# Kernel optimization log

Measured on AMD Instinct MI355X. Metric: run time of the kernel, lower is better.

## Reference

```python
import jax, jax.numpy as jnp
import numpy as np

N_NODES = 100000
N_EDGES = 3200000
D = 32


def _gat(x, edge_index, W, att_s, att_d, bias, heads, ch, neg_slope):
    """PyG-style GATConv (shared lin for src/dst, add_self_loops=False).
    x: [N, D_in], edge_index: [2, E], W: [heads*ch, D_in],
    att_s/att_d: [heads, ch], bias: [heads*ch]. Returns [N, heads*ch]."""
    n = x.shape[0]
    h = (x @ W.T).reshape(n, heads, ch)                      # [N,H,C]
    a_s = (h * att_s[None]).sum(-1)                           # [N,H]
    a_d = (h * att_d[None]).sum(-1)                           # [N,H]
    src, dst = edge_index[0], edge_index[1]
    logits = jax.nn.leaky_relu(a_s[src] + a_d[dst], neg_slope)  # [E,H]
    # segment softmax over edges grouped by destination node
    m = jax.ops.segment_max(logits, dst, num_segments=n)     # [N,H]
    m = jnp.where(jnp.isfinite(m), m, 0.0)                    # nodes w/ no in-edges
    ex = jnp.exp(logits - m[dst])                             # [E,H]
    denom = jax.ops.segment_sum(ex, dst, num_segments=n)     # [N,H]
    alpha = ex / (denom[dst] + 1e-16)                         # [E,H]
    out = jax.ops.segment_sum(alpha[:, :, None] * h[src], dst, num_segments=n)  # [N,H,C]
    return out.reshape(n, heads * ch) + bias


def setup_inputs() -> dict:
    key = jax.random.key(0)
    ks = jax.random.split(key, 16)
    x = jax.random.normal(ks[0], (N_NODES, D), dtype=jnp.float32)
    edge_index = jax.random.randint(ks[1], (2, N_EDGES), 0, N_NODES, dtype=jnp.int64)
    s = 1.0 / np.sqrt(D)
    return {
        "x": x,
        "edge_index": edge_index,
        "W1": jax.random.normal(ks[2], (32, D), dtype=jnp.float32) * s,
        "att_s1": jax.random.normal(ks[3], (2, 16), dtype=jnp.float32) * 0.05,
        "att_d1": jax.random.normal(ks[4], (2, 16), dtype=jnp.float32) * 0.05,
        "b1": jnp.full((32,), 0.1, dtype=jnp.float32),
        "ea1": jnp.ones((1,), dtype=jnp.float32),  # edge_activator
        "W2": jax.random.normal(ks[5], (32, 32), dtype=jnp.float32) * s,
        "att_s2": jax.random.normal(ks[6], (2, 16), dtype=jnp.float32) * 0.05,
        "att_d2": jax.random.normal(ks[7], (2, 16), dtype=jnp.float32) * 0.05,
        "b2": jnp.full((32,), 0.1, dtype=jnp.float32),
        "W3": jax.random.normal(ks[8], (32, 32), dtype=jnp.float32) * s,
        "att_s3": jax.random.normal(ks[9], (1, 32), dtype=jnp.float32) * 0.05,
        "att_d3": jax.random.normal(ks[10], (1, 32), dtype=jnp.float32) * 0.05,
        "b3": jnp.full((32,), 0.1, dtype=jnp.float32),
    }


def reference(x, edge_index, W1, att_s1, att_d1, b1, ea1,
              W2, att_s2, att_d2, b2, W3, att_s3, att_d3, b3):
    # --- layer 1 (negative_slope=0.01) ---
    h = _gat(x, edge_index, W1, att_s1, att_d1, b1, heads=2, ch=16, neg_slope=0.01)
    scale = jnp.tanh(ea1)[0]
    scale = jnp.where(scale < 0.1, 1.0, scale)  # 'continue' branch skips the scaling
    h = h * scale
    h = h + 0.05 * jax.lax.stop_gradient(h)      # h + 0.05*h.detach()
    h = jax.nn.elu(h)                            # eval path (training=False)
    h = jnp.clip(h, -3.0, 3.0)
    # --- layer 2 (default negative_slope=0.2) ---
    h = _gat(h, edge_index, W2, att_s2, att_d2, b2, heads=2, ch=16, neg_slope=0.2)
    h = jax.nn.elu(h)
    h = jnp.clip(h, -3.0, 3.0)
    # --- layer 3: heads=1, concat=False ---
    out = _gat(h, edge_index, W3, att_s3, att_d3, b3, heads=1, ch=32, neg_slope=0.2)
    return out
```

## Files before the change

kernel.cpp:

```cpp
#include <hip/hip_runtime.h>
#include <hip/hip_bf16.h>
#include <hip/hip_fp16.h>


#define NPB  128
#define CAPB 6144
#define PAD_SENTINEL 0xFFFFFFFFu

template <int H, int NL>
__device__ __forceinline__ void transform_body(
    const float* __restrict__ in, const float* __restrict__ W,
    const float* __restrict__ att_s, const float* __restrict__ att_d,
    __half* __restrict__ h16, float* __restrict__ a_s, float* __restrict__ a_d,
    int node0, int nlim, float (*Wl)[33], float (*xs)[32]) {
    constexpr int C = 32 / H;
    constexpr int NTH = NL * 32;
    int t = threadIdx.x;
    for (int i = t; i < 1024; i += NTH) Wl[i >> 5][i & 31] = W[i];
    int nl = t >> 5, o = t & 31;
    int node = node0 + nl;
    xs[nl][o] = (node < nlim) ? in[(size_t)node * 32 + o] : 0.f;
    __syncthreads();
    float acc = 0.f;
#pragma unroll
    for (int k = 0; k < 32; k++) acc = fmaf(xs[nl][k], Wl[o][k], acc);
    if (node < nlim) {
        h16[(size_t)node * 32 + o] = __float2half_rn(acc);
        float vs = acc * att_s[o];
        float vd = acc * att_d[o];
#pragma unroll
        for (int m = C / 2; m >= 1; m >>= 1) {
            vs += __shfl_xor(vs, m, 64);
            vd += __shfl_xor(vd, m, 64);
        }
        if ((o % C) == 0) {
            int hh = o / C;
            a_s[node * H + hh] = vs;
            a_d[node * H + hh] = vd;
        }
    }
}

__global__ void __launch_bounds__(1024)
k_bin_t1(const int* __restrict__ src, const int* __restrict__ dst,
         int* __restrict__ bucket_cursor, unsigned int* __restrict__ pairs,
         int e, int nb, int nbb,
         const float* __restrict__ in, const float* __restrict__ W,
         const float* __restrict__ att_s, const float* __restrict__ att_d,
         __half* __restrict__ h16, float* __restrict__ a_s,
         float* __restrict__ a_d, int nsplit) {
    __shared__ union {
        struct { int h[1024]; int bs[1024]; int cb[1024]; unsigned int stage[8192]; } b;
        struct { float Wl[32][33]; float xs[32][32]; } t;
    } sh;
    int t = threadIdx.x;
    if ((int)blockIdx.x >= nbb) {
        int node0 = ((int)blockIdx.x - nbb) * 32;
        transform_body<2, 32>(in, W, att_s, att_d, h16, a_s, a_d,
                              node0, nsplit, sh.t.Wl, sh.t.xs);
        return;
    }
    sh.b.h[t] = 0;
    __syncthreads();
    int e4 = e >> 2;
    int base4 = blockIdx.x * 2048;
    int boff[8];
    unsigned int pk[8];
#pragma unroll
    for (int k = 0; k < 2; k++) {
        int i4 = base4 + k * 1024 + t;
        if (i4 < e4) {
            int4 dv = ((const int4*)dst)[i4];
            int4 sv = ((const int4*)src)[i4];
            const int* dd = (const int*)&dv;
            const int* ss = (const int*)&sv;
#pragma unroll
            for (int j = 0; j < 4; j++) {
                int q = 4 * k + j;
                int d = dd[j];
                int b = d >> 7;
                pk[q] = ((unsigned int)ss[j] << 7) | (unsigned int)(d & 127);
                int off = atomicAdd(&sh.b.h[b], 1);
                boff[q] = (b << 16) | off;
            }
        } else {
#pragma unroll
            for (int j = 0; j < 4; j++) boff[4 * k + j] = -1;
        }
    }
    __syncthreads();
    if (t >= 128 && t - 128 < nb) {
        int b = t - 128;
        int c = sh.b.h[b];
        sh.b.cb[b] = c ? atomicAdd(&bucket_cursor[b], c) : 0;
    }
    if (t < 64) {
        int sum = 0;
#pragma unroll
        for (int j = 0; j < 16; j++) sum += sh.b.h[t * 16 + j];
        int run = sum;
#pragma unroll
        for (int off = 1; off < 64; off <<= 1) {
            int v = __shfl_up(run, off, 64);
            if (t >= off) run += v;
        }
        int base = run - sum;
#pragma unroll
        for (int j = 0; j < 16; j++) {
            int b = t * 16 + j;
            sh.b.bs[b] = base;
            base += sh.b.h[b];
        }
    }
    __syncthreads();
#pragma unroll
    for (int q = 0; q < 8; q++) {
        if (boff[q] >= 0) {
            int b = boff[q] >> 16;
            sh.b.stage[sh.b.bs[b] + (boff[q] & 0xFFFF)] = pk[q];
        }
    }
    __syncthreads();
    int wv = t >> 6, ln = t & 63;
    for (int b = wv; b < nb; b += 16) {
        int c = sh.b.h[b];
        if (c == 0) continue;
        int gb = sh.b.cb[b];
        int room = CAPB - gb;
        if (c > room) c = (room > 0) ? room : 0;
        unsigned int* dp = pairs + (size_t)b * CAPB + gb;
        const unsigned int* sp = sh.b.stage + sh.b.bs[b];
        for (int o = ln; o < c; o += 64) dp[o] = sp[o];
    }
    if (blockIdx.x == 0 && t < (e & 3)) {
        int i = (e & ~3) + t;
        int d = dst[i];
        int b = d >> 7;
        int r = atomicAdd(&bucket_cursor[b], 1);
        if (r < CAPB)
            pairs[(size_t)b * CAPB + r] =
                ((unsigned int)src[i] << 7) | (unsigned int)(d & 127);
    }
}

__global__ void __launch_bounds__(512)
k_sort_t1(const unsigned int* __restrict__ pairs,
          const int* __restrict__ bucket_cursor,
          int2* __restrict__ rowinfo, int* __restrict__ src_sorted,
          int n, int nb,
          const float* __restrict__ in, const float* __restrict__ W,
          const float* __restrict__ att_s, const float* __restrict__ att_d,
          __half* __restrict__ h16, float* __restrict__ a_s,
          float* __restrict__ a_d, int nsplit) {
    __shared__ union {
        struct { int cnt[NPB]; int cur[NPB]; int total;
                 unsigned int lp[CAPB]; int op[CAPB]; } s;
        struct { float Wl[32][33]; float xs[16][32]; } t;
    } sh;
    int t = threadIdx.x;
    if ((int)blockIdx.x >= nb) {
        int node0 = nsplit + ((int)blockIdx.x - nb) * 16;
        transform_body<2, 16>(in, W, att_s, att_d, h16, a_s, a_d,
                              node0, n, sh.t.Wl, sh.t.xs);
        return;
    }
    int b = blockIdx.x;
    int bbase = b * CAPB;
    int m = bucket_cursor[b];
    if (m > CAPB) m = CAPB;
    if (t < NPB) sh.s.cnt[t] = 0;
    __syncthreads();
    for (int cb = 0; cb < m; cb += 4096) {
        unsigned int pv[8];
#pragma unroll
        for (int u = 0; u < 8; u++) {
            int i = cb + u * 512 + t;
            pv[u] = (i < m) ? pairs[bbase + i] : PAD_SENTINEL;
        }
#pragma unroll
        for (int u = 0; u < 8; u++) {
            int i = cb + u * 512 + t;
            if (i < m) sh.s.lp[i] = pv[u];
            if (pv[u] != PAD_SENTINEL) atomicAdd(&sh.s.cnt[pv[u] & 127], 1);
        }
    }
    __syncthreads();
    if (t < 64) {
        int c0 = sh.s.cnt[2 * t];
        int c1 = sh.s.cnt[2 * t + 1];
        int sum = c0 + c1;
        int run = sum;
#pragma unroll
        for (int off = 1; off < 64; off <<= 1) {
            int v = __shfl_up(run, off, 64);
            if (t >= off) run += v;
        }
        int ex = run - sum;
        sh.s.cur[2 * t] = ex;
        sh.s.cur[2 * t + 1] = ex + c0;
        int node = b * NPB + 2 * t;
        if (node < n) rowinfo[node] = make_int2(bbase + ex, c0);
        if (node + 1 < n) rowinfo[node + 1] = make_int2(bbase + ex + c0, c1);
        if (t == 63) sh.s.total = run;
    }
    __syncthreads();
    for (int cb = 0; cb < m; cb += 4096) {
        unsigned int pv[8];
        int of[8];
#pragma unroll
        for (int u = 0; u < 8; u++) {
            int i = cb + u * 512 + t;
            pv[u] = (i < m) ? sh.s.lp[i] : PAD_SENTINEL;
        }
#pragma unroll
        for (int u = 0; u < 8; u++)
            if (pv[u] != PAD_SENTINEL) of[u] = atomicAdd(&sh.s.cur[pv[u] & 127], 1);
#pragma unroll
        for (int u = 0; u < 8; u++)
            if (pv[u] != PAD_SENTINEL) sh.s.op[of[u]] = (int)(pv[u] >> 7);
    }
    __syncthreads();
    int nt4 = (sh.s.total + 3) >> 2;
    int4* dst4 = (int4*)(src_sorted + bbase);
    const int4* src4 = (const int4*)sh.s.op;
    for (int i = t; i < nt4; i += 512) dst4[i] = src4[i];
}

template <int H>
__global__ void k_transform(const float* __restrict__ in, const float* __restrict__ W,
                            const float* __restrict__ att_s, const float* __restrict__ att_d,
                            __half* __restrict__ h16, float* __restrict__ a_s,
                            float* __restrict__ a_d, int n) {
    __shared__ float Wl[32][33];
    __shared__ float xs[8][32];
    transform_body<H, 8>(in, W, att_s, att_d, h16, a_s, a_d,
                         blockIdx.x * 8, n, Wl, xs);
}

template <int H, int EPI>
__global__ void k_edge(const int2* __restrict__ rowinfo, const int* __restrict__ src_sorted,
                       const __half* __restrict__ h16,
                       const float* __restrict__ a_s, const float* __restrict__ a_d,
                       const float* __restrict__ bias, const float* __restrict__ ea,
                       float* __restrict__ out, int n, float slope) {
    constexpr int CAP = 128;
    constexpr int RSTR = 2 * CAP + 16;
    __shared__ int lds_raw[8][H][RSTR];
    int nw = threadIdx.x >> 5;
    int hl = threadIdx.x & 31;
    int node = blockIdx.x * 8 + nw;
    if (node >= n) return;
    int2 bi = rowinfo[node];
    int beg = bi.x, deg = bi.y;
    int padB = (deg + 15) & ~15;

    float ad[H];
#pragma unroll
    for (int hh = 0; hh < H; hh++) ad[hh] = a_d[node * H + hh];

    float ds[H];
#pragma unroll
    for (int hh = 0; hh < H; hh++) ds[hh] = 0.f;
    bool fast = (padB <= CAP);
    if (fast) {
        for (int idx = hl; idx < padB; idx += 32) {
            if (idx < deg) {
                int s = src_sorted[beg + idx];
                if (H == 2) {
                    float2 as2 = *(const float2*)((const char*)a_s + (unsigned)(s << 3));
                    float l0 = as2.x + ad[0]; l0 = fmaxf(l0, l0 * slope);
                    float l1 = as2.y + ad[1]; l1 = fmaxf(l1, l1 * slope);
                    float e0 = __expf(l0), e1 = __expf(l1);
                    ds[0] += e0; ds[1] += e1;
                    ((int2*)lds_raw[nw][0])[idx] = make_int2(s, __float_as_int(e0));
                    ((int2*)lds_raw[nw][H - 1])[idx] = make_int2(s, __float_as_int(e1));
                } else {
                    float l0 = a_s[s] + ad[0]; l0 = fmaxf(l0, l0 * slope);
                    float e0 = __expf(l0);
                    ds[0] += e0;
                    ((int2*)lds_raw[nw][0])[idx] = make_int2(s, __float_as_int(e0));
                }
            } else {
#pragma unroll
                for (int hh = 0; hh < H; hh++)
                    ((int2*)lds_raw[nw][hh])[idx] = make_int2(0, 0);
            }
        }
    } else {
        for (int idx = hl; idx < deg; idx += 32) {
            int s = src_sorted[beg + idx];
            if (H == 2) {
                float2 as2 = *(const float2*)((const char*)a_s + (unsigned)(s << 3));
                float l0 = as2.x + ad[0]; l0 = fmaxf(l0, l0 * slope);
                float l1 = as2.y + ad[1]; l1 = fmaxf(l1, l1 * slope);
                ds[0] += __expf(l0); ds[1] += __expf(l1);
            } else {
                float l0 = a_s[s] + ad[0]; l0 = fmaxf(l0, l0 * slope);
                ds[0] += __expf(l0);
            }
        }
    }

    int e2 = hl >> 4;
    int l16 = hl & 15;
    int hd = (H == 2) ? (l16 >> 3) : 0;
    int co = l16 << 2;
    float adh = ad[hd];
    float acc0 = 0.f, acc1 = 0.f;
    const char* hbase = (const char*)h16;
    const int* lb = &lds_raw[nw][hd][e2 * 4];

    if (fast) {
        for (int base = 0; base < padB; base += 16) {
            int4 qa = *(const int4*)(lb + base * 2);
            int4 qb = *(const int4*)(lb + base * 2 + 8);
            int4 qc = *(const int4*)(lb + base * 2 + 16);
            int4 qd = *(const int4*)(lb + base * 2 + 24);
            __half2 h0 = *(const __half2*)(hbase + (unsigned)((qa.x << 6) + co));
            __half2 h1 = *(const __half2*)(hbase + (unsigned)((qa.z << 6) + co));
            __half2 h2 = *(const __half2*)(hbase + (unsigned)((qb.x << 6) + co));
            __half2 h3 = *(const __half2*)(hbase + (unsigned)((qb.z << 6) + co));
            __half2 h4 = *(const __half2*)(hbase + (unsigned)((qc.x << 6) + co));
            __half2 h5 = *(const __half2*)(hbase + (unsigned)((qc.z << 6) + co));
            __half2 h6 = *(const __half2*)(hbase + (unsigned)((qd.x << 6) + co));
            __half2 h7 = *(const __half2*)(hbase + (unsigned)((qd.z << 6) + co));
            float xa0 = __int_as_float(qa.y), xa1 = __int_as_float(qa.w);
            float xb0 = __int_as_float(qb.y), xb1 = __int_as_float(qb.w);
            float xc0 = __int_as_float(qc.y), xc1 = __int_as_float(qc.w);
            float xd0 = __int_as_float(qd.y), xd1 = __int_as_float(qd.w);
            acc0 = fmaf(xa0, __half2float(__low2half(h0)), acc0);
            acc1 = fmaf(xa0, __half2float(__high2half(h0)), acc1);
            acc0 = fmaf(xa1, __half2float(__low2half(h1)), acc0);
            acc1 = fmaf(xa1, __half2float(__high2half(h1)), acc1);
            acc0 = fmaf(xb0, __half2float(__low2half(h2)), acc0);
            acc1 = fmaf(xb0, __half2float(__high2half(h2)), acc1);
            acc0 = fmaf(xb1, __half2float(__low2half(h3)), acc0);
            acc1 = fmaf(xb1, __half2float(__high2half(h3)), acc1);
            acc0 = fmaf(xc0, __half2float(__low2half(h4)), acc0);
            acc1 = fmaf(xc0, __half2float(__high2half(h4)), acc1);
            acc0 = fmaf(xc1, __half2float(__low2half(h5)), acc0);
            acc1 = fmaf(xc1, __half2float(__high2half(h5)), acc1);
            acc0 = fmaf(xd0, __half2float(__low2half(h6)), acc0);
            acc1 = fmaf(xd0, __half2float(__high2half(h6)), acc1);
            acc0 = fmaf(xd1, __half2float(__low2half(h7)), acc0);
            acc1 = fmaf(xd1, __half2float(__high2half(h7)), acc1);
        }
    } else {
        for (int base = 0; base < deg; base += 16) {
#pragma unroll
            for (int u = 0; u < 8; u++) {
                int idx = base + u * 2 + e2;
                int s = 0;
                float ex = 0.f;
                if (idx < deg) {
                    s = src_sorted[beg + idx];
                    float l = a_s[s * H + hd] + adh;
                    l = fmaxf(l, l * slope);
                    ex = __expf(l);
                }
                __half2 hv = *(const __half2*)(hbase + (unsigned)((s << 6) + co));
                acc0 = fmaf(ex, __half2float(__low2half(hv)), acc0);
                acc1 = fmaf(ex, __half2float(__high2half(hv)), acc1);
            }
        }
    }

#pragma unroll
    for (int hh = 0; hh < H; hh++) {
        float v = ds[hh];
#pragma unroll
        for (int m = 16; m >= 1; m >>= 1) v += __shfl_xor(v, m, 64);
        ds[hh] = 1.f / (v + 1e-16f);
    }

    acc0 += __shfl_xor(acc0, 16, 64);
    acc1 += __shfl_xor(acc1, 16, 64);

    if (l16 == hl) {
        float invd = ds[hd];
        float2 bv = *(const float2*)(bias + l16 * 2);
        float v0 = fmaf(acc0, invd, bv.x);
        float v1 = fmaf(acc1, invd, bv.y);
        if (EPI == 1) {
            float s0 = tanhf(ea[0]);
            if (s0 < 0.1f) s0 = 1.0f;
            s0 *= 1.05f;
            v0 *= s0; v1 *= s0;
            v0 = (v0 > 0.f) ? v0 : expm1f(v0);
            v1 = (v1 > 0.f) ? v1 : expm1f(v1);
            v0 = fminf(3.f, fmaxf(-3.f, v0));
            v1 = fminf(3.f, fmaxf(-3.f, v1));
        } else if (EPI == 2) {
            v0 = (v0 > 0.f) ? v0 : expm1f(v0);
            v1 = (v1 > 0.f) ? v1 : expm1f(v1);
            v0 = fminf(3.f, fmaxf(-3.f, v0));
            v1 = fminf(3.f, fmaxf(-3.f, v1));
        }
        *(float2*)(out + (size_t)node * 32 + l16 * 2) = make_float2(v0, v1);
    }
}

extern "C" void kernel_launch(void* const* d_in, const int* in_sizes, int n_in,
                              void* d_out, int out_size, void* d_ws, size_t ws_size,
                              hipStream_t stream) {
    const float* x   = (const float*)d_in[0];
    const int*   ei  = (const int*)d_in[1];
    const float* W1  = (const float*)d_in[2];
    const float* as1 = (const float*)d_in[3];
    const float* ad1 = (const float*)d_in[4];
    const float* b1  = (const float*)d_in[5];
    const float* ea1 = (const float*)d_in[6];
    const float* W2  = (const float*)d_in[7];
    const float* as2 = (const float*)d_in[8];
    const float* ad2 = (const float*)d_in[9];
    const float* b2  = (const float*)d_in[10];
    const float* W3  = (const float*)d_in[11];
    const float* as3 = (const float*)d_in[12];
    const float* ad3 = (const float*)d_in[13];
    const float* b3  = (const float*)d_in[14];
    float* out = (float*)d_out;

    const int n = in_sizes[0] / 32;
    const int e = in_sizes[1] / 2;
    const int* src = ei;
    const int* dst = ei + e;
    const int nb = (n + NPB - 1) / NPB;

    char* w = (char*)d_ws;
    auto alloc = [&](size_t bytes) -> void* {
        void* p = (void*)w;
        w += (bytes + 255) & ~(size_t)255;
        return p;
    };
    __half* h16     = (__half*)alloc((size_t)n * 32 * 2);
    float* a_s      = (float*)alloc((size_t)n * 2 * 4);
    float* a_d      = (float*)alloc((size_t)n * 2 * 4);
    float* bufA     = (float*)alloc((size_t)n * 32 * 4);
    float* bufB     = (float*)alloc((size_t)n * 32 * 4);
    int2* rowinfo   = (int2*)alloc((size_t)n * 8);
    int* bucket_cur = (int*)alloc((size_t)(nb + 1) * 4);
    int* src_sorted = (int*)alloc((size_t)nb * CAPB * 4);
    unsigned int* pairs = (unsigned int*)bufA;

    int nsplit = n / 2;
    nsplit = (nsplit + 31) & ~31;
    if (nsplit > n) nsplit = n;
    const int t1a = (nsplit + 31) / 32;
    const int t1b = (n - nsplit + 15) / 16;
    int e4 = e >> 2;
    const int nbb = (e4 + 2047) / 2048;

    hipMemsetAsync(bucket_cur, 0, (size_t)nb * 4, stream);
    k_bin_t1<<<nbb + t1a, 1024, 0, stream>>>(src, dst, bucket_cur, pairs, e, nb, nbb,
                                             x, W1, as1, ad1, h16, a_s, a_d, nsplit);
    k_sort_t1<<<nb + t1b, 512, 0, stream>>>(pairs, bucket_cur, rowinfo, src_sorted, n, nb,
                                            x, W1, as1, ad1, h16, a_s, a_d, nsplit);

    const int tgrid = (n + 7) / 8;
    const int egrid = (n + 7) / 8;

    k_edge<2, 1><<<egrid, 256, 0, stream>>>(rowinfo, src_sorted, h16, a_s, a_d, b1, ea1, bufA, n, 0.01f);

    k_transform<2><<<tgrid, 256, 0, stream>>>(bufA, W2, as2, ad2, h16, a_s, a_d, n);
    k_edge<2, 2><<<egrid, 256, 0, stream>>>(rowinfo, src_sorted, h16, a_s, a_d, b2, nullptr, bufB, n, 0.2f);

    k_transform<1><<<tgrid, 256, 0, stream>>>(bufB, W3, as3, ad3, h16, a_s, a_d, n);
    k_edge<1, 0><<<egrid, 256, 0, stream>>>(rowinfo, src_sorted, h16, a_s, a_d, b3, nullptr, out, n, 0.2f);
}
```

Before: 335.6 us.

## Fuse next-layer linear transform into edge aggregation epilogue

```diff
diff --git a/kernel.cpp b/kernel.cpp
--- a/kernel.cpp
+++ b/kernel.cpp
@@ -226,30 +226,29 @@
     for (int i = t; i < nt4; i += 512) dst4[i] = src4[i];
 }
 
-template <int H>
-__global__ void k_transform(const float* __restrict__ in, const float* __restrict__ W,
-                            const float* __restrict__ att_s, const float* __restrict__ att_d,
-                            __half* __restrict__ h16, float* __restrict__ a_s,
-                            float* __restrict__ a_d, int n) {
-    __shared__ float Wl[32][33];
-    __shared__ float xs[8][32];
-    transform_body<H, 8>(in, W, att_s, att_d, h16, a_s, a_d,
-                         blockIdx.x * 8, n, Wl, xs);
-}
-
-template <int H, int EPI>
-__global__ void k_edge(const int2* __restrict__ rowinfo, const int* __restrict__ src_sorted,
-                       const __half* __restrict__ h16,
-                       const float* __restrict__ a_s, const float* __restrict__ a_d,
-                       const float* __restrict__ bias, const float* __restrict__ ea,
-                       float* __restrict__ out, int n, float slope) {
+template <int H, int EPI, int H2>
+__global__ void __launch_bounds__(256)
+k_edge_f(const int2* __restrict__ rowinfo, const int* __restrict__ src_sorted,
+         const __half* __restrict__ h16,
+         const float* __restrict__ a_s, const float* __restrict__ a_d,
+         const float* __restrict__ bias, const float* __restrict__ ea,
+         const float* __restrict__ Wn, const float* __restrict__ att_sn,
+         const float* __restrict__ att_dn,
+         __half* __restrict__ h16n, float* __restrict__ a_sn,
+         float* __restrict__ a_dn, int n, float slope) {
     constexpr int CAP = 128;
     constexpr int RSTR = 2 * CAP + 16;
     __shared__ int lds_raw[8][H][RSTR];
-    int nw = threadIdx.x >> 5;
-    int hl = threadIdx.x & 31;
+    __shared__ float Wl2[32][33];
+    __shared__ float row[8][32];
+    int t = threadIdx.x;
+    for (int i = t; i < 1024; i += 256) Wl2[i >> 5][i & 31] = Wn[i];
+    __syncthreads();
+    int nw = t >> 5;
+    int hl = t & 31;
     int node = blockIdx.x * 8 + nw;
     if (node >= n) return;
+    float ats = att_sn[hl], atd = att_dn[hl];
     int2 bi = rowinfo[node];
     int beg = bi.x, deg = bi.y;
     int padB = (deg + 15) & ~15;
@@ -372,7 +371,182 @@
         for (int m = 16; m >= 1; m >>= 1) v += __shfl_xor(v, m, 64);
         ds[hh] = 1.f / (v + 1e-16f);
     }
-
+    acc0 += __shfl_xor(acc0, 16, 64);
+    acc1 += __shfl_xor(acc1, 16, 64);
+
+    float invd = ds[hd];
+    float2 bv = *(const float2*)(bias + l16 * 2);
+    float v0 = fmaf(acc0, invd, bv.x);
+    float v1 = fmaf(acc1, invd, bv.y);
+    if (EPI == 1) {
+        float s0 = tanhf(ea[0]);
+        if (s0 < 0.1f) s0 = 1.0f;
+        s0 *= 1.05f;
+        v0 *= s0; v1 *= s0;
+    }
+    v0 = (v0 > 0.f) ? v0 : expm1f(v0);
+    v1 = (v1 > 0.f) ? v1 : expm1f(v1);
+    v0 = fminf(3.f, fmaxf(-3.f, v0));
+    v1 = fminf(3.f, fmaxf(-3.f, v1));
+
+    if (hl < 16) {
+        row[nw][2 * l16] = v0;
+        row[nw][2 * l16 + 1] = v1;
+    }
+    float acc = 0.f;
+#pragma unroll
+    for (int k = 0; k < 32; k++) acc = fmaf(row[nw][k], Wl2[hl][k], acc);
+    h16n[(size_t)node * 32 + hl] = __float2half_rn(acc);
+    float vs = acc * ats;
+    float vd = acc * atd;
+    constexpr int C2 = 32 / H2;
+#pragma unroll
+    for (int m = C2 / 2; m >= 1; m >>= 1) {
+        vs += __shfl_xor(vs, m, 64);
+        vd += __shfl_xor(vd, m, 64);
+    }
+    if ((hl % C2) == 0) {
+        int hh = hl / C2;
+        a_sn[node * H2 + hh] = vs;
+        a_dn[node * H2 + hh] = vd;
+    }
+}
+
+template <int H, int EPI>
+__global__ void k_edge(const int2* __restrict__ rowinfo, const int* __restrict__ src_sorted,
+                       const __half* __restrict__ h16,
+                       const float* __restrict__ a_s, const float* __restrict__ a_d,
+                       const float* __restrict__ bias, const float* __restrict__ ea,
+                       float* __restrict__ out, int n, float slope) {
+    constexpr int CAP = 128;
+    constexpr int RSTR = 2 * CAP + 16;
+    __shared__ int lds_raw[8][H][RSTR];
+    int nw = threadIdx.x >> 5;
+    int hl = threadIdx.x & 31;
+    int node = blockIdx.x * 8 + nw;
+    if (node >= n) return;
+    int2 bi = rowinfo[node];
+    int beg = bi.x, deg = bi.y;
+    int padB = (deg + 15) & ~15;
+
+    float ad[H];
+#pragma unroll
+    for (int hh = 0; hh < H; hh++) ad[hh] = a_d[node * H + hh];
+
+    float ds[H];
+#pragma unroll
+    for (int hh = 0; hh < H; hh++) ds[hh] = 0.f;
+    bool fast = (padB <= CAP);
+    if (fast) {
+        for (int idx = hl; idx < padB; idx += 32) {
+            if (idx < deg) {
+                int s = src_sorted[beg + idx];
+                if (H == 2) {
+                    float2 as2 = *(const float2*)((const char*)a_s + (unsigned)(s << 3));
+                    float l0 = as2.x + ad[0]; l0 = fmaxf(l0, l0 * slope);
+                    float l1 = as2.y + ad[1]; l1 = fmaxf(l1, l1 * slope);
+                    float e0 = __expf(l0), e1 = __expf(l1);
+                    ds[0] += e0; ds[1] += e1;
+                    ((int2*)lds_raw[nw][0])[idx] = make_int2(s, __float_as_int(e0));
+                    ((int2*)lds_raw[nw][H - 1])[idx] = make_int2(s, __float_as_int(e1));
+                } else {
+                    float l0 = a_s[s] + ad[0]; l0 = fmaxf(l0, l0 * slope);
+                    float e0 = __expf(l0);
+                    ds[0] += e0;
+                    ((int2*)lds_raw[nw][0])[idx] = make_int2(s, __float_as_int(e0));
+                }
+            } else {
+#pragma unroll
+                for (int hh = 0; hh < H; hh++)
+                    ((int2*)lds_raw[nw][hh])[idx] = make_int2(0, 0);
+            }
+        }
+    } else {
+        for (int idx = hl; idx < deg; idx += 32) {
+            int s = src_sorted[beg + idx];
+            if (H == 2) {
+                float2 as2 = *(const float2*)((const char*)a_s + (unsigned)(s << 3));
+                float l0 = as2.x + ad[0]; l0 = fmaxf(l0, l0 * slope);
+                float l1 = as2.y + ad[1]; l1 = fmaxf(l1, l1 * slope);
+                ds[0] += __expf(l0); ds[1] += __expf(l1);
+            } else {
+                float l0 = a_s[s] + ad[0]; l0 = fmaxf(l0, l0 * slope);
+                ds[0] += __expf(l0);
+            }
+        }
+    }
+
+    int e2 = hl >> 4;
+    int l16 = hl & 15;
+    int hd = (H == 2) ? (l16 >> 3) : 0;
+    int co = l16 << 2;
+    float adh = ad[hd];
+    float acc0 = 0.f, acc1 = 0.f;
+    const char* hbase = (const char*)h16;
+    const int* lb = &lds_raw[nw][hd][e2 * 4];
+
+    if (fast) {
+        for (int base = 0; base < padB; base += 16) {
+            int4 qa = *(const int4*)(lb + base * 2);
+            int4 qb = *(const int4*)(lb + base * 2 + 8);
+            int4 qc = *(const int4*)(lb + base * 2 + 16);
+            int4 qd = *(const int4*)(lb + base * 2 + 24);
+            __half2 h0 = *(const __half2*)(hbase + (unsigned)((qa.x << 6) + co));
+            __half2 h1 = *(const __half2*)(hbase + (unsigned)((qa.z << 6) + co));
+            __half2 h2 = *(const __half2*)(hbase + (unsigned)((qb.x << 6) + co));
+            __half2 h3 = *(const __half2*)(hbase + (unsigned)((qb.z << 6) + co));
+            __half2 h4 = *(const __half2*)(hbase + (unsigned)((qc.x << 6) + co));
+            __half2 h5 = *(const __half2*)(hbase + (unsigned)((qc.z << 6) + co));
+            __half2 h6 = *(const __half2*)(hbase + (unsigned)((qd.x << 6) + co));
+            __half2 h7 = *(const __half2*)(hbase + (unsigned)((qd.z << 6) + co));
+            float xa0 = __int_as_float(qa.y), xa1 = __int_as_float(qa.w);
+            float xb0 = __int_as_float(qb.y), xb1 = __int_as_float(qb.w);
+            float xc0 = __int_as_float(qc.y), xc1 = __int_as_float(qc.w);
+            float xd0 = __int_as_float(qd.y), xd1 = __int_as_float(qd.w);
+            acc0 = fmaf(xa0, __half2float(__low2half(h0)), acc0);
+            acc1 = fmaf(xa0, __half2float(__high2half(h0)), acc1);
+            acc0 = fmaf(xa1, __half2float(__low2half(h1)), acc0);
+            acc1 = fmaf(xa1, __half2float(__high2half(h1)), acc1);
+            acc0 = fmaf(xb0, __half2float(__low2half(h2)), acc0);
+            acc1 = fmaf(xb0, __half2float(__high2half(h2)), acc1);
+            acc0 = fmaf(xb1, __half2float(__low2half(h3)), acc0);
+            acc1 = fmaf(xb1, __half2float(__high2half(h3)), acc1);
+            acc0 = fmaf(xc0, __half2float(__low2half(h4)), acc0);
+            acc1 = fmaf(xc0, __half2float(__high2half(h4)), acc1);
+            acc0 = fmaf(xc1, __half2float(__low2half(h5)), acc0);
+            acc1 = fmaf(xc1, __half2float(__high2half(h5)), acc1);
+            acc0 = fmaf(xd0, __half2float(__low2half(h6)), acc0);
+            acc1 = fmaf(xd0, __half2float(__high2half(h6)), acc1);
+            acc0 = fmaf(xd1, __half2float(__low2half(h7)), acc0);
+            acc1 = fmaf(xd1, __half2float(__high2half(h7)), acc1);
+        }
+    } else {
+        for (int base = 0; base < deg; base += 16) {
+#pragma unroll
+            for (int u = 0; u < 8; u++) {
+                int idx = base + u * 2 + e2;
+                int s = 0;
+                float ex = 0.f;
+                if (idx < deg) {
+                    s = src_sorted[beg + idx];
+                    float l = a_s[s * H + hd] + adh;
+                    l = fmaxf(l, l * slope);
+                    ex = __expf(l);
+                }
+                __half2 hv = *(const __half2*)(hbase + (unsigned)((s << 6) + co));
+                acc0 = fmaf(ex, __half2float(__low2half(hv)), acc0);
+                acc1 = fmaf(ex, __half2float(__high2half(hv)), acc1);
+            }
+        }
+    }
+
+#pragma unroll
+    for (int hh = 0; hh < H; hh++) {
+        float v = ds[hh];
+#pragma unroll
+        for (int m = 16; m >= 1; m >>= 1) v += __shfl_xor(v, m, 64);
+        ds[hh] = 1.f / (v + 1e-16f);
+    }
     acc0 += __shfl_xor(acc0, 16, 64);
     acc1 += __shfl_xor(acc1, 16, 64);
 
@@ -432,15 +606,25 @@
         w += (bytes + 255) & ~(size_t)255;
         return p;
     };
-    __half* h16     = (__half*)alloc((size_t)n * 32 * 2);
-    float* a_s      = (float*)alloc((size_t)n * 2 * 4);
-    float* a_d      = (float*)alloc((size_t)n * 2 * 4);
-    float* bufA     = (float*)alloc((size_t)n * 32 * 4);
-    float* bufB     = (float*)alloc((size_t)n * 32 * 4);
+    __half* h16a    = (__half*)alloc((size_t)n * 32 * 2);
+    float* a_s1     = (float*)alloc((size_t)n * 2 * 4);
+    float* a_d1     = (float*)alloc((size_t)n * 2 * 4);
     int2* rowinfo   = (int2*)alloc((size_t)n * 8);
     int* bucket_cur = (int*)alloc((size_t)(nb + 1) * 4);
     int* src_sorted = (int*)alloc((size_t)nb * CAPB * 4);
-    unsigned int* pairs = (unsigned int*)bufA;
+    unsigned int* pairs = (unsigned int*)alloc((size_t)nb * CAPB * 4);
+
+    char* sc = (char*)pairs;
+    auto carve = [&](size_t bytes) -> void* {
+        void* p = (void*)sc;
+        sc += (bytes + 255) & ~(size_t)255;
+        return p;
+    };
+    __half* h16b = (__half*)carve((size_t)n * 32 * 2);
+    float* a_s2  = (float*)carve((size_t)n * 2 * 4);
+    float* a_d2  = (float*)carve((size_t)n * 2 * 4);
+    float* a_s3  = (float*)carve((size_t)n * 4);
+    float* a_d3  = (float*)carve((size_t)n * 4);
 
     int nsplit = n / 2;
     nsplit = (nsplit + 31) & ~31;
@@ -452,18 +636,18 @@
 
     hipMemsetAsync(bucket_cur, 0, (size_t)nb * 4, stream);
     k_bin_t1<<<nbb + t1a, 1024, 0, stream>>>(src, dst, bucket_cur, pairs, e, nb, nbb,
-                                             x, W1, as1, ad1, h16, a_s, a_d, nsplit);
+                                             x, W1, as1, ad1, h16a, a_s1, a_d1, nsplit);
     k_sort_t1<<<nb + t1b, 512, 0, stream>>>(pairs, bucket_cur, rowinfo, src_sorted, n, nb,
-                                            x, W1, as1, ad1, h16, a_s, a_d, nsplit);
-
-    const int tgrid = (n + 7) / 8;
+                                            x, W1, as1, ad1, h16a, a_s1, a_d1, nsplit);
+
     const int egrid = (n + 7) / 8;
 
-    k_edge<2, 1><<<egrid, 256, 0, stream>>>(rowinfo, src_sorted, h16, a_s, a_d, b1, ea1, bufA, n, 0.01f);
-
-    k_transform<2><<<tgrid, 256, 0, stream>>>(bufA, W2, as2, ad2, h16, a_s, a_d, n);
-    k_edge<2, 2><<<egrid, 256, 0, stream>>>(rowinfo, src_sorted, h16, a_s, a_d, b2, nullptr, bufB, n, 0.2f);
-
-    k_transform<1><<<tgrid, 256, 0, stream>>>(bufB, W3, as3, ad3, h16, a_s, a_d, n);
-    k_edge<1, 0><<<egrid, 256, 0, stream>>>(rowinfo, src_sorted, h16, a_s, a_d, b3, nullptr, out, n, 0.2f);
+    k_edge_f<2, 1, 2><<<egrid, 256, 0, stream>>>(rowinfo, src_sorted, h16a, a_s1, a_d1,
+                                                 b1, ea1, W2, as2, ad2,
+                                                 h16b, a_s2, a_d2, n, 0.01f);
+    k_edge_f<2, 2, 1><<<egrid, 256, 0, stream>>>(rowinfo, src_sorted, h16b, a_s2, a_d2,
+                                                 b2, nullptr, W3, as3, ad3,
+                                                 h16a, a_s3, a_d3, n, 0.2f);
+    k_edge<1, 0><<<egrid, 256, 0, stream>>>(rowinfo, src_sorted, h16a, a_s3, a_d3,
+                                            b3, nullptr, out, n, 0.2f);
 }
```

Result: faster. 318.5 us (-5.1%).
